# Kernel optimization log

Hardware: AMD Instinct MI355X
Metric: run time of the kernel (lower is better)

Reference implementation:

```python
import jax, jax.numpy as jnp
import numpy as np

N = 2048       # x_dim (input features)
M = 2048       # y_dim (output features)
R0 = 1024      # components in table 0 (knn table)
D_K = 1024     # key encoder embed dim
D_V = 1024     # val encoder embed dim
BATCH = 512
ISTA_ALPHA = 1.0
ISTA_MAXITER = 5


def _ortho_encoder(key, n, d):
    # get_embedding_matrix with ortho=True: QR of (s,s) gaussian, take [:n,:d]
    s = max(n, d)
    q = jnp.linalg.qr(jax.random.normal(key, (s, s), dtype=jnp.float32))[0]
    return q[:n, :d]


def setup_inputs() -> dict:
    key = jax.random.key(0)
    kw, kk, kv, kx = jax.random.split(key, 4)
    W = jax.random.normal(kw, (N, M), dtype=jnp.float32) / np.float32(np.sqrt(N))
    # torch: V, S, U = svd(W); U = U.T  -> V = left vecs (n,k), U = right vecs (m,k)
    Usvd, S, Vh = jnp.linalg.svd(W, full_matrices=False)
    V = Usvd          # (n, k)
    Ur = Vh.T         # (m, k)
    key_enc = _ortho_encoder(kk, N, D_K)   # (n, d_k)
    val_enc = _ortho_encoder(kv, M, D_V)   # (m, d_v)
    # table 0: knn table over components [0:R0]
    keys_t0 = V[:, :R0].T @ key_enc        # (R0, d_k)
    vals_t0 = Ur[:, :R0].T @ val_enc       # (R0, d_v)
    scales_t0 = S[:R0][:, None]            # (R0, 1)
    # table 1: plain low-rank table over components [R0:]
    keys_t1 = V[:, R0:]                    # (n, R1)
    vals_t1 = Ur[:, R0:]                   # (m, R1)
    scales_t1 = S[R0:][:, None]            # (R1, 1)
    x = jax.random.normal(kx, (BATCH, N), dtype=jnp.float32)
    return {"x": x, "key_enc": key_enc, "val_enc": val_enc,
            "keys_t0": keys_t0, "vals_t0": vals_t0, "scales_t0": scales_t0,
            "keys_t1": keys_t1, "vals_t1": vals_t1, "scales_t1": scales_t1}


def _soft(x, t):
    return jnp.sign(x) * jnp.maximum(jnp.abs(x) - t, 0.0)


def reference(x, key_enc, val_enc, keys_t0, vals_t0, scales_t0,
              keys_t1, vals_t1, scales_t1):
    # --- table 0: knn path (batched; original looped over batch samples) ---
    q = x @ key_enc                        # (B, d_k)
    alphas = q @ keys_t0.T                 # (B, R0)
    betas = alphas * scales_t0.T           # (B, R0)
    yb = betas @ vals_t0                   # (B, d_v)
    # ISTA: min ||yb - z @ val_enc||^2 + alpha*||z||_1, step=1 (val_enc has
    # orthonormal columns so Lipschitz const of grad is 1)
    z = yb @ val_enc.T                     # z0, (B, m)
    for _ in range(ISTA_MAXITER):
        z = _soft(z + (yb - z @ val_enc) @ val_enc.T, ISTA_ALPHA)
    y = z                                  # knn path assigns y[b,:] = yh
    # --- table 1: low-rank path (accumulates) ---
    alphas2 = x @ keys_t1                  # (B, R1)
    betas2 = alphas2 * scales_t1.T         # (B, R1)
    y = y + betas2 @ vals_t1.T             # (B, m)
    return y
```

## Files before the change

kernel.cpp:

```cpp
#include <hip/hip_runtime.h>


typedef _Float16 f16x8 __attribute__((ext_vector_type(8)));
typedef _Float16 f16x4 __attribute__((ext_vector_type(4)));
typedef float f32x4 __attribute__((ext_vector_type(4)));

enum { EPI_H, EPI_QOFF, EPI_SPLIT, EPI_SOFT, EPI_ZQ, EPI_ZQF, EPI_FINAL };

typedef const __attribute__((address_space(1))) void* gas_ptr;
typedef __attribute__((address_space(3))) void* las_ptr;

__device__ __forceinline__ void gload16(const void* g, void* l) {
  __builtin_amdgcn_global_load_lds((gas_ptr)g, (las_ptr)l, 16, 0, 0);
}

__device__ __forceinline__ float softt(float t) {
  float s = fabsf(t) - 1.0f;
  s = s > 0.0f ? s : 0.0f;
  return copysignf(s, t);
}

__global__ __launch_bounds__(256) void convAll(
    const float* __restrict__ e0, const float* __restrict__ e1,
    const float* __restrict__ e2, const float* __restrict__ e3,
    _Float16* __restrict__ o0, _Float16* __restrict__ o1,
    _Float16* __restrict__ o2, _Float16* __restrict__ o3,
    const float* __restrict__ s1, const float* __restrict__ s2,
    const float4* __restrict__ pa, f16x4* __restrict__ qa, int na,
    const float4* __restrict__ pb, f16x4* __restrict__ qb, int nb,
    const float4* __restrict__ pc, f16x4* __restrict__ qc, int nc) {
  const int z = blockIdx.z;
  if (z == 4) {
    const int total = na + nb + nc;
    const int bid = blockIdx.y * 32 + blockIdx.x;
    const int nthr = 2048 * 256;
    for (int i = bid * 256 + threadIdx.y * 32 + threadIdx.x; i < total;
         i += nthr) {
      const float4* s;
      f16x4* d;
      int j = i;
      if (j < na) {
        s = pa; d = qa;
      } else if ((j -= na) < nb) {
        s = pb; d = qb;
      } else {
        j -= nb; s = pc; d = qc;
      }
      float4 v = s[j];
      f16x4 h = {(_Float16)v.x, (_Float16)v.y, (_Float16)v.z, (_Float16)v.w};
      d[j] = h;
    }
    return;
  }
  const float* in = z == 0 ? e0 : z == 1 ? e1 : z == 2 ? e2 : e3;
  _Float16* out = z == 0 ? o0 : z == 1 ? o1 : z == 2 ? o2 : o3;
  const int R = (z < 2) ? 2048 : 1024;
  const int C = 1024;
  const int mode = z == 1 ? 1 : z == 2 ? 2 : 0;
  const float* sv = z == 1 ? s1 : s2;
  __shared__ float t[32][33];
  const int tx = threadIdx.x, ty = threadIdx.y;
  const int c0 = blockIdx.x * 32, r0 = blockIdx.y * 32;
  if (r0 >= R) return;
#pragma unroll
  for (int i = 0; i < 32; i += 8)
    t[ty + i][tx] = in[(size_t)(r0 + ty + i) * C + c0 + tx];
  __syncthreads();
#pragma unroll
  for (int i = 0; i < 32; i += 8) {
    float v = t[tx][ty + i];
    if (mode == 1) v *= sv[c0 + ty + i];
    if (mode == 2) v *= sv[r0 + tx];
    out[(size_t)(c0 + ty + i) * R + r0 + tx] = (_Float16)v;
  }
}

template <int EPI>
__device__ __forceinline__ void gtile(
    const _Float16* __restrict__ A, int lda, const _Float16* __restrict__ B,
    int ldb, int nK, int N, int brow, int bcol, const float* __restrict__ dgv,
    float* __restrict__ dgout, float* __restrict__ fA, float* __restrict__ fB,
    _Float16* __restrict__ oh, _Float16* __restrict__ oh2,
    float* __restrict__ ofin, _Float16* sm, int tid) {
  const int lane = tid & 63;
  const int w = tid >> 6;
  const int wr = w & 1;
  const int wk = w >> 1;
  const int srow = lane >> 3;
  const int scol = ((lane & 7) ^ srow) << 3;
  const int a15 = lane & 15;
  const int hi = lane >> 4;
  const int l7 = lane & 7;

  const _Float16* apg = A + (size_t)(brow + (w << 4) + srow) * lda + scol;
  const _Float16* bpg = B + (size_t)(bcol + (w << 4) + srow) * ldb + scol;
  _Float16* AB = sm;
  _Float16* BB = sm + 16384;
  const int ldstA = w << 10;

  const int ca = ((wk << 2) + hi) ^ l7;
  int raddr[2], baddr[4];
#pragma unroll
  for (int mi = 0; mi < 2; ++mi)
    raddr[mi] = ((wr << 5) + (mi << 4) + a15) * 64 + (ca << 3);
#pragma unroll
  for (int ni = 0; ni < 4; ++ni)
    baddr[ni] = ((ni << 4) + a15) * 64 + (ca << 3);

  f32x4 acc[2][4] = {};

  __syncthreads();

#pragma unroll
  for (int p = 0; p < 2; ++p) {
    gload16(apg + p * 64, AB + p * 4096 + ldstA);
    gload16(apg + p * 64 + (size_t)8 * lda, AB + p * 4096 + ldstA + 512);
    gload16(bpg + p * 64, BB + p * 4096 + ldstA);
    gload16(bpg + p * 64 + (size_t)8 * ldb, BB + p * 4096 + ldstA + 512);
  }

  for (int kt = 0; kt < nK; ++kt) {
    if (kt + 2 < nK) {
      const int bf = (kt + 2) & 3;
      const int co = (kt + 2) << 6;
      gload16(apg + co, AB + bf * 4096 + ldstA);
      gload16(apg + co + (size_t)8 * lda, AB + bf * 4096 + ldstA + 512);
      gload16(bpg + co, BB + bf * 4096 + ldstA);
      gload16(bpg + co + (size_t)8 * ldb, BB + bf * 4096 + ldstA + 512);
    }
    const int rem = nK - 1 - kt;
    if (rem >= 2)
      asm volatile("s_waitcnt vmcnt(8)" ::: "memory");
    else if (rem == 1)
      asm volatile("s_waitcnt vmcnt(4)" ::: "memory");
    else
      asm volatile("s_waitcnt vmcnt(0)" ::: "memory");
    __builtin_amdgcn_s_barrier();
    __builtin_amdgcn_sched_barrier(0);
    const _Float16* Ab = AB + (kt & 3) * 4096;
    const _Float16* Bb = BB + (kt & 3) * 4096;
    f16x8 av[2], bv[4];
    av[0] = *(const f16x8*)(Ab + raddr[0]);
    av[1] = *(const f16x8*)(Ab + raddr[1]);
    bv[0] = *(const f16x8*)(Bb + baddr[0]);
    bv[1] = *(const f16x8*)(Bb + baddr[1]);
    bv[2] = *(const f16x8*)(Bb + baddr[2]);
    bv[3] = *(const f16x8*)(Bb + baddr[3]);
#pragma unroll
    for (int mi = 0; mi < 2; ++mi)
#pragma unroll
      for (int ni = 0; ni < 4; ++ni)
        acc[mi][ni] = __builtin_amdgcn_mfma_f32_16x16x32_f16(
            av[mi], bv[ni], acc[mi][ni], 0, 0, 0);
  }

  __syncthreads();
  float* scr = (float*)sm;
  const int sl = (wr << 6) + lane;
  if (wk == 1) {
#pragma unroll
    for (int mi = 0; mi < 2; ++mi)
#pragma unroll
      for (int ni = 0; ni < 4; ++ni)
#pragma unroll
        for (int r = 0; r < 4; ++r)
          scr[(((mi << 2) + ni) * 4 + r) * 128 + sl] = acc[mi][ni][r];
  }
  __syncthreads();
  if (wk == 0) {
#pragma unroll
    for (int mi = 0; mi < 2; ++mi) {
#pragma unroll
      for (int ni = 0; ni < 4; ++ni) {
#pragma unroll
        for (int r = 0; r < 4; ++r) {
          const float v =
              acc[mi][ni][r] + scr[(((mi << 2) + ni) * 4 + r) * 128 + sl];
          const int row = brow + (wr << 5) + (mi << 4) + (hi << 2) + r;
          const int col = bcol + (ni << 4) + a15;
          const size_t idx = (size_t)row * N + col;
          if constexpr (EPI == EPI_H) {
            oh[idx] = (_Float16)v;
          } else if constexpr (EPI == EPI_QOFF) {
            if (row == col) {
              dgout[row] = 1.0f - v;
              oh[idx] = (_Float16)0.0f;
            } else {
              oh[idx] = (_Float16)(-v);
            }
          } else if constexpr (EPI == EPI_SPLIT) {
            if (col < 1024)
              oh[(size_t)row * 1024 + col] = (_Float16)v;
            else
              oh2[(size_t)row * 1024 + (col - 1024)] = (_Float16)v;
          } else if constexpr (EPI == EPI_SOFT) {
            fA[idx] = v;
            float s = softt(v);
            fB[idx] = s;
            oh[idx] = (_Float16)s;
          } else if constexpr (EPI == EPI_ZQ) {
            float t = fA[idx] + dgv[col] * fB[idx] + v;
            float s = softt(t);
            fB[idx] = s;
            oh[idx] = (_Float16)s;
          } else if constexpr (EPI == EPI_ZQF) {
            float t = fA[idx] + dgv[col] * fB[idx] + v;
            fB[idx] = softt(t);
          } else {
            ofin[idx] = fB[idx] + v;
          }
        }
      }
    }
  }
}

struct WS {
  const _Float16 *ve, *vt1, *w0pT_r, *Bcat, *qoff_r, *x, *kt0s, *vt0T, *w0_r,
      *q_r, *be2;
  _Float16 *w0pT_w, *qoff_w, *w0_w, *q_w, *be2_w, *zhA, *zhB;
  float *z0, *zf, *dg;
};

__global__ __launch_bounds__(256, 2) void kD2(WS p) {
  __shared__ __align__(16) _Float16 sm[32768];
  const int tid = threadIdx.x;
  const int bid = blockIdx.x;
  if (bid < 1024) {
    gtile<EPI_QOFF>(p.ve, 1024, p.ve, 1024, 16, 2048, (bid >> 5) << 6,
                    (bid & 31) << 6, nullptr, p.dg, nullptr, nullptr, p.qoff_w,
                    nullptr, nullptr, sm, tid);
  } else if (bid < 1280) {
    const int i = bid - 1024;
    gtile<EPI_SPLIT>(p.x, 2048, p.Bcat, 2048, 32, 2048, (i >> 5) << 6,
                     (i & 31) << 6, nullptr, nullptr, nullptr, nullptr, p.q_w,
                     p.be2_w, nullptr, sm, tid);
  } else {
    const int i = bid - 1280;
    gtile<EPI_H>(p.kt0s, 1024, p.vt0T, 1024, 16, 1024, (i >> 4) << 6,
                 (i & 15) << 6, nullptr, nullptr, nullptr, nullptr, p.w0_w,
                 nullptr, nullptr, sm, tid);
  }
}

__global__ __launch_bounds__(256, 2) void kW0p(WS p) {
  __shared__ __align__(16) _Float16 sm[32768];
  const int bid = blockIdx.x;
  gtile<EPI_H>(p.ve, 1024, p.w0_r, 1024, 16, 1024, (bid >> 4) << 6,
               (bid & 15) << 6, nullptr, nullptr, nullptr, nullptr, p.w0pT_w,
               nullptr, nullptr, sm, threadIdx.x);
}

__global__ __launch_bounds__(256, 2) void kC2(WS p) {
  __shared__ __align__(16) _Float16 sm[32768];
  const int bid = blockIdx.x;
  gtile<EPI_SOFT>(p.q_r, 1024, p.w0pT_r, 1024, 16, 2048, (bid >> 5) << 6,
                  (bid & 31) << 6, nullptr, nullptr, p.z0, p.zf, p.zhA,
                  nullptr, nullptr, sm, threadIdx.x);
}

template <bool AB>
__global__ __launch_bounds__(256, 2) void kZQ(WS p) {
  __shared__ __align__(16) _Float16 sm[32768];
  const int bid = blockIdx.x;
  gtile<EPI_ZQ>(AB ? p.zhA : p.zhB, 2048, p.qoff_r, 2048, 32, 2048,
                (bid >> 5) << 6, (bid & 31) << 6, p.dg, nullptr, p.z0, p.zf,
                AB ? p.zhB : p.zhA, nullptr, nullptr, sm, threadIdx.x);
}

__global__ __launch_bounds__(256, 2) void kZQF(WS p, float* out) {
  __shared__ __align__(16) _Float16 sm[32768];
  const int bid = blockIdx.x;
  const int brow = (bid >> 5) << 6, bcol = (bid & 31) << 6;
  gtile<EPI_ZQF>(p.zhB, 2048, p.qoff_r, 2048, 32, 2048, brow, bcol, p.dg,
                 nullptr, p.z0, p.zf, nullptr, nullptr, nullptr, sm,
                 threadIdx.x);
  gtile<EPI_FINAL>(p.be2, 1024, p.vt1, 1024, 16, 2048, brow, bcol, nullptr,
                   nullptr, nullptr, p.zf, nullptr, nullptr, out, sm,
                   threadIdx.x);
}

extern "C" void kernel_launch(void* const* d_in, const int* in_sizes, int n_in,
                              void* d_out, int out_size, void* d_ws,
                              size_t ws_size, hipStream_t stream) {
  const float* x = (const float*)d_in[0];
  const float* key_enc = (const float*)d_in[1];
  const float* val_enc = (const float*)d_in[2];
  const float* keys_t0 = (const float*)d_in[3];
  const float* vals_t0 = (const float*)d_in[4];
  const float* scales_t0 = (const float*)d_in[5];
  const float* keys_t1 = (const float*)d_in[6];
  const float* vals_t1 = (const float*)d_in[7];
  const float* scales_t1 = (const float*)d_in[8];

  constexpr size_t M1 = 1048576;
  _Float16* ws = (_Float16*)d_ws;
  _Float16* ve_h = ws;
  _Float16* vt1_h = ws + 2 * M1;
  _Float16* w0pT = ws + 4 * M1;
  _Float16* Bcat = ws + 6 * M1;
  _Float16* zhA = ws + 6 * M1;
  float* z0_f = (float*)(ws + 7 * M1);
  _Float16* zhB = ws + 9 * M1;
  _Float16* qoff = ws + 10 * M1;
  _Float16* x_h = ws + 14 * M1;
  _Float16* kt0s = ws + 15 * M1;
  float* z_f = (float*)(ws + 15 * M1);
  _Float16* vt0T = ws + 16 * M1;
  _Float16* w0 = ws + 17 * M1;
  _Float16* q_h = ws + 18 * M1;
  _Float16* be2 = ws + 18 * M1 + 524288;
  float* dg = (float*)(ws + 19 * M1);

  WS p;
  p.ve = ve_h; p.vt1 = vt1_h; p.w0pT_r = w0pT; p.w0pT_w = w0pT;
  p.Bcat = Bcat; p.qoff_r = qoff; p.qoff_w = qoff; p.x = x_h;
  p.kt0s = kt0s; p.vt0T = vt0T; p.w0_r = w0; p.w0_w = w0;
  p.q_r = q_h; p.q_w = q_h; p.be2 = be2; p.be2_w = be2;
  p.zhA = zhA; p.zhB = zhB; p.z0 = z0_f; p.zf = z_f; p.dg = dg;

  convAll<<<dim3(32, 64, 5), dim3(32, 8), 0, stream>>>(
      key_enc, keys_t1, keys_t0, vals_t0, Bcat, Bcat + 2 * M1, kt0s, vt0T,
      scales_t1, scales_t0, (const float4*)x, (f16x4*)x_h, 262144,
      (const float4*)val_enc, (f16x4*)ve_h, 524288, (const float4*)vals_t1,
      (f16x4*)vt1_h, 524288);
  kD2<<<1536, 256, 0, stream>>>(p);
  kW0p<<<512, 256, 0, stream>>>(p);
  kC2<<<256, 256, 0, stream>>>(p);
  kZQ<true><<<256, 256, 0, stream>>>(p);
  kZQ<false><<<256, 256, 0, stream>>>(p);
  kZQ<true><<<256, 256, 0, stream>>>(p);
  kZQF<<<256, 256, 0, stream>>>(p, (float*)d_out);
}
```

Baseline: 120.7 us.

## Replace precomputed Gram and weight products with factored low-rank ISTA chain

```diff
diff --git a/kernel.cpp b/kernel.cpp
--- a/kernel.cpp
+++ b/kernel.cpp
@@ -5,7 +5,7 @@
 typedef _Float16 f16x4 __attribute__((ext_vector_type(4)));
 typedef float f32x4 __attribute__((ext_vector_type(4)));
 
-enum { EPI_H, EPI_QOFF, EPI_SPLIT, EPI_SOFT, EPI_ZQ, EPI_ZQF, EPI_FINAL };
+enum { EPI_SPLIT, EPI_BH, EPI_YP, EPI_SOFT, EPI_ZUP, EPI_ZUPF };
 
 typedef const __attribute__((address_space(1))) void* gas_ptr;
 typedef __attribute__((address_space(3))) void* las_ptr;
@@ -21,193 +21,177 @@
 }
 
 __global__ __launch_bounds__(256) void convAll(
-    const float* __restrict__ e0, const float* __restrict__ e1,
-    const float* __restrict__ e2, const float* __restrict__ e3,
-    _Float16* __restrict__ o0, _Float16* __restrict__ o1,
-    _Float16* __restrict__ o2, _Float16* __restrict__ o3,
-    const float* __restrict__ s1, const float* __restrict__ s2,
-    const float4* __restrict__ pa, f16x4* __restrict__ qa, int na,
-    const float4* __restrict__ pb, f16x4* __restrict__ qb, int nb,
-    const float4* __restrict__ pc, f16x4* __restrict__ qc, int nc) {
+    const float* __restrict__ ke, const float* __restrict__ k1,
+    const float* __restrict__ v0, const float* __restrict__ ve,
+    _Float16* __restrict__ oKe, _Float16* __restrict__ oK1,
+    _Float16* __restrict__ oV0, _Float16* __restrict__ oVeT,
+    const float* __restrict__ s1, const float* __restrict__ s0,
+    const float4* __restrict__ px, f16x4* __restrict__ qx,
+    const float4* __restrict__ pve, f16x4* __restrict__ qve,
+    const float4* __restrict__ pv1, f16x4* __restrict__ qv1,
+    const float4* __restrict__ pk0, f16x4* __restrict__ qk0) {
   const int z = blockIdx.z;
   if (z == 4) {
-    const int total = na + nb + nc;
+    const int n_x = 262144, n_ve = 524288, n_v1 = 524288, n_k0 = 262144;
+    const int total = n_x + n_ve + n_v1 + n_k0;
     const int bid = blockIdx.y * 32 + blockIdx.x;
-    const int nthr = 2048 * 256;
     for (int i = bid * 256 + threadIdx.y * 32 + threadIdx.x; i < total;
-         i += nthr) {
+         i += 2048 * 256) {
+      int j = i;
       const float4* s;
       f16x4* d;
-      int j = i;
-      if (j < na) {
-        s = pa; d = qa;
-      } else if ((j -= na) < nb) {
-        s = pb; d = qb;
+      float sc = 1.0f;
+      if (j < n_x) {
+        s = px; d = qx;
+      } else if ((j -= n_x) < n_ve) {
+        s = pve; d = qve;
+      } else if ((j -= n_ve) < n_v1) {
+        s = pv1; d = qv1;
       } else {
-        j -= nb; s = pc; d = qc;
+        j -= n_v1; s = pk0; d = qk0; sc = s0[j >> 8];
       }
       float4 v = s[j];
-      f16x4 h = {(_Float16)v.x, (_Float16)v.y, (_Float16)v.z, (_Float16)v.w};
+      f16x4 h = {(_Float16)(v.x * sc), (_Float16)(v.y * sc),
+                 (_Float16)(v.z * sc), (_Float16)(v.w * sc)};
       d[j] = h;
     }
     return;
   }
-  const float* in = z == 0 ? e0 : z == 1 ? e1 : z == 2 ? e2 : e3;
-  _Float16* out = z == 0 ? o0 : z == 1 ? o1 : z == 2 ? o2 : o3;
-  const int R = (z < 2) ? 2048 : 1024;
-  const int C = 1024;
-  const int mode = z == 1 ? 1 : z == 2 ? 2 : 0;
-  const float* sv = z == 1 ? s1 : s2;
+  const float* in = z == 0 ? ke : z == 1 ? k1 : z == 2 ? v0 : ve;
+  _Float16* out = z == 0 ? oKe : z == 1 ? oK1 : z == 2 ? oV0 : oVeT;
+  const int R = (z == 2) ? 1024 : 2048;
+  const int mode = (z == 1) ? 1 : 0;
   __shared__ float t[32][33];
   const int tx = threadIdx.x, ty = threadIdx.y;
   const int c0 = blockIdx.x * 32, r0 = blockIdx.y * 32;
   if (r0 >= R) return;
 #pragma unroll
   for (int i = 0; i < 32; i += 8)
-    t[ty + i][tx] = in[(size_t)(r0 + ty + i) * C + c0 + tx];
+    t[ty + i][tx] = in[(size_t)(r0 + ty + i) * 1024 + c0 + tx];
   __syncthreads();
 #pragma unroll
   for (int i = 0; i < 32; i += 8) {
     float v = t[tx][ty + i];
-    if (mode == 1) v *= sv[c0 + ty + i];
-    if (mode == 2) v *= sv[r0 + tx];
+    if (mode == 1) v *= s1[c0 + ty + i];
     out[(size_t)(c0 + ty + i) * R + r0 + tx] = (_Float16)v;
   }
 }
 
 template <int EPI>
-__device__ __forceinline__ void gtile(
+__device__ __forceinline__ void gt32(
     const _Float16* __restrict__ A, int lda, const _Float16* __restrict__ B,
-    int ldb, int nK, int N, int brow, int bcol, const float* __restrict__ dgv,
-    float* __restrict__ dgout, float* __restrict__ fA, float* __restrict__ fB,
-    _Float16* __restrict__ oh, _Float16* __restrict__ oh2,
+    int ldb, int nK, int N, int brow, int bcol, float* __restrict__ fA,
+    float* __restrict__ fB, _Float16* __restrict__ oh,
+    _Float16* __restrict__ oh2, const float* __restrict__ fC,
     float* __restrict__ ofin, _Float16* sm, int tid) {
   const int lane = tid & 63;
   const int w = tid >> 6;
-  const int wr = w & 1;
+  const int wc = w & 1;
   const int wk = w >> 1;
   const int srow = lane >> 3;
   const int scol = ((lane & 7) ^ srow) << 3;
-  const int a15 = lane & 15;
-  const int hi = lane >> 4;
-  const int l7 = lane & 7;
-
-  const _Float16* apg = A + (size_t)(brow + (w << 4) + srow) * lda + scol;
+  const int a15 = lane & 15, hi = lane >> 4, l7 = lane & 7;
+
+  const _Float16* apg = A + (size_t)(brow + (w << 3) + srow) * lda + scol;
   const _Float16* bpg = B + (size_t)(bcol + (w << 4) + srow) * ldb + scol;
   _Float16* AB = sm;
-  _Float16* BB = sm + 16384;
-  const int ldstA = w << 10;
-
+  _Float16* BB = sm + 8192;
   const int ca = ((wk << 2) + hi) ^ l7;
-  int raddr[2], baddr[4];
+  int raddr[2], baddr[2];
 #pragma unroll
   for (int mi = 0; mi < 2; ++mi)
-    raddr[mi] = ((wr << 5) + (mi << 4) + a15) * 64 + (ca << 3);
-#pragma unroll
-  for (int ni = 0; ni < 4; ++ni)
-    baddr[ni] = ((ni << 4) + a15) * 64 + (ca << 3);
-
-  f32x4 acc[2][4] = {};
-
+    raddr[mi] = ((mi << 4) + a15) * 64 + (ca << 3);
+#pragma unroll
+  for (int ni = 0; ni < 2; ++ni)
+    baddr[ni] = ((wc << 5) + (ni << 4) + a15) * 64 + (ca << 3);
+
+  f32x4 acc[2][2] = {};
   __syncthreads();
 
 #pragma unroll
   for (int p = 0; p < 2; ++p) {
-    gload16(apg + p * 64, AB + p * 4096 + ldstA);
-    gload16(apg + p * 64 + (size_t)8 * lda, AB + p * 4096 + ldstA + 512);
-    gload16(bpg + p * 64, BB + p * 4096 + ldstA);
-    gload16(bpg + p * 64 + (size_t)8 * ldb, BB + p * 4096 + ldstA + 512);
-  }
-
+    gload16(apg + p * 64, AB + p * 2048 + (w << 9));
+    gload16(bpg + p * 64, BB + p * 4096 + (w << 10));
+    gload16(bpg + p * 64 + (size_t)8 * ldb, BB + p * 4096 + (w << 10) + 512);
+  }
   for (int kt = 0; kt < nK; ++kt) {
     if (kt + 2 < nK) {
       const int bf = (kt + 2) & 3;
       const int co = (kt + 2) << 6;
-      gload16(apg + co, AB + bf * 4096 + ldstA);
-      gload16(apg + co + (size_t)8 * lda, AB + bf * 4096 + ldstA + 512);
-      gload16(bpg + co, BB + bf * 4096 + ldstA);
-      gload16(bpg + co + (size_t)8 * ldb, BB + bf * 4096 + ldstA + 512);
+      gload16(apg + co, AB + bf * 2048 + (w << 9));
+      gload16(bpg + co, BB + bf * 4096 + (w << 10));
+      gload16(bpg + co + (size_t)8 * ldb, BB + bf * 4096 + (w << 10) + 512);
     }
     const int rem = nK - 1 - kt;
     if (rem >= 2)
-      asm volatile("s_waitcnt vmcnt(8)" ::: "memory");
+      asm volatile("s_waitcnt vmcnt(6)" ::: "memory");
     else if (rem == 1)
-      asm volatile("s_waitcnt vmcnt(4)" ::: "memory");
+      asm volatile("s_waitcnt vmcnt(3)" ::: "memory");
     else
       asm volatile("s_waitcnt vmcnt(0)" ::: "memory");
     __builtin_amdgcn_s_barrier();
     __builtin_amdgcn_sched_barrier(0);
-    const _Float16* Ab = AB + (kt & 3) * 4096;
+    const _Float16* Ab = AB + (kt & 3) * 2048;
     const _Float16* Bb = BB + (kt & 3) * 4096;
-    f16x8 av[2], bv[4];
+    f16x8 av[2], bv[2];
     av[0] = *(const f16x8*)(Ab + raddr[0]);
     av[1] = *(const f16x8*)(Ab + raddr[1]);
     bv[0] = *(const f16x8*)(Bb + baddr[0]);
     bv[1] = *(const f16x8*)(Bb + baddr[1]);
-    bv[2] = *(const f16x8*)(Bb + baddr[2]);
-    bv[3] = *(const f16x8*)(Bb + baddr[3]);
 #pragma unroll
     for (int mi = 0; mi < 2; ++mi)
 #pragma unroll
-      for (int ni = 0; ni < 4; ++ni)
+      for (int ni = 0; ni < 2; ++ni)
         acc[mi][ni] = __builtin_amdgcn_mfma_f32_16x16x32_f16(
             av[mi], bv[ni], acc[mi][ni], 0, 0, 0);
   }
-
   __syncthreads();
   float* scr = (float*)sm;
-  const int sl = (wr << 6) + lane;
+  const int sl = (wc << 6) + lane;
   if (wk == 1) {
 #pragma unroll
     for (int mi = 0; mi < 2; ++mi)
 #pragma unroll
-      for (int ni = 0; ni < 4; ++ni)
+      for (int ni = 0; ni < 2; ++ni)
 #pragma unroll
         for (int r = 0; r < 4; ++r)
-          scr[(((mi << 2) + ni) * 4 + r) * 128 + sl] = acc[mi][ni][r];
+          scr[(((mi << 1) + ni) * 4 + r) * 128 + sl] = acc[mi][ni][r];
   }
   __syncthreads();
   if (wk == 0) {
 #pragma unroll
     for (int mi = 0; mi < 2; ++mi) {
 #pragma unroll
-      for (int ni = 0; ni < 4; ++ni) {
+      for (int ni = 0; ni < 2; ++ni) {
 #pragma unroll
         for (int r = 0; r < 4; ++r) {
           const float v =
-              acc[mi][ni][r] + scr[(((mi << 2) + ni) * 4 + r) * 128 + sl];
-          const int row = brow + (wr << 5) + (mi << 4) + (hi << 2) + r;
-          const int col = bcol + (ni << 4) + a15;
+              acc[mi][ni][r] + scr[(((mi << 1) + ni) * 4 + r) * 128 + sl];
+          const int row = brow + (mi << 4) + (hi << 2) + r;
+          const int col = bcol + (wc << 5) + (ni << 4) + a15;
           const size_t idx = (size_t)row * N + col;
-          if constexpr (EPI == EPI_H) {
-            oh[idx] = (_Float16)v;
-          } else if constexpr (EPI == EPI_QOFF) {
-            if (row == col) {
-              dgout[row] = 1.0f - v;
-              oh[idx] = (_Float16)0.0f;
-            } else {
-              oh[idx] = (_Float16)(-v);
-            }
-          } else if constexpr (EPI == EPI_SPLIT) {
+          if constexpr (EPI == EPI_SPLIT) {
             if (col < 1024)
               oh[(size_t)row * 1024 + col] = (_Float16)v;
             else
               oh2[(size_t)row * 1024 + (col - 1024)] = (_Float16)v;
+          } else if constexpr (EPI == EPI_BH) {
+            oh[idx] = (_Float16)v;
+          } else if constexpr (EPI == EPI_YP) {
+            ofin[idx] = v;
           } else if constexpr (EPI == EPI_SOFT) {
             fA[idx] = v;
             float s = softt(v);
             fB[idx] = s;
             oh[idx] = (_Float16)s;
-          } else if constexpr (EPI == EPI_ZQ) {
-            float t = fA[idx] + dgv[col] * fB[idx] + v;
+          } else if constexpr (EPI == EPI_ZUP) {
+            float t = fA[idx] + fB[idx] - v;
             float s = softt(t);
             fB[idx] = s;
             oh[idx] = (_Float16)s;
-          } else if constexpr (EPI == EPI_ZQF) {
-            float t = fA[idx] + dgv[col] * fB[idx] + v;
-            fB[idx] = softt(t);
           } else {
-            ofin[idx] = fB[idx] + v;
+            float t = fA[idx] + fB[idx] - v;
+            ofin[idx] = fC[idx] + softt(t);
           }
         }
       }
@@ -216,68 +200,93 @@
 }
 
 struct WS {
-  const _Float16 *ve, *vt1, *w0pT_r, *Bcat, *qoff_r, *x, *kt0s, *vt0T, *w0_r,
-      *q_r, *be2;
-  _Float16 *w0pT_w, *qoff_w, *w0_w, *q_w, *be2_w, *zhA, *zhB;
-  float *z0, *zf, *dg;
+  const _Float16 *ve, *veT, *vt1, *Bcat, *x, *k0r, *vt0T, *q_r, *be2_r,
+      *bet_r, *yb_r;
+  _Float16 *q_w, *be2_w, *bet_w, *yb_w, *c_w, *zhA, *zhB;
+  const _Float16* c_r;
+  float *z0, *zf, *yp;
 };
 
-__global__ __launch_bounds__(256, 2) void kD2(WS p) {
-  __shared__ __align__(16) _Float16 sm[32768];
-  const int tid = threadIdx.x;
+__device__ __forceinline__ void map512(int b, int& br, int& bc) {
+  const int x = b & 7, i = b >> 3;
+  bc = (x << 2) | (i & 3);
+  br = i >> 2;
+}
+__device__ __forceinline__ void map256(int b, int& br, int& bc) {
+  const int x = b & 7, i = b >> 3;
+  bc = (x << 1) | (i & 1);
+  br = i >> 1;
+}
+
+__global__ __launch_bounds__(256, 2) void kC1(WS p) {
+  __shared__ __align__(16) _Float16 sm[24576];
+  int br, bc;
+  map512(blockIdx.x, br, bc);
+  gt32<EPI_SPLIT>(p.x, 2048, p.Bcat, 2048, 32, 2048, br << 5, bc << 6,
+                  nullptr, nullptr, p.q_w, p.be2_w, nullptr, nullptr, sm,
+                  threadIdx.x);
+}
+
+__global__ __launch_bounds__(256, 2) void kBYP(WS p) {
+  __shared__ __align__(16) _Float16 sm[24576];
   const int bid = blockIdx.x;
-  if (bid < 1024) {
-    gtile<EPI_QOFF>(p.ve, 1024, p.ve, 1024, 16, 2048, (bid >> 5) << 6,
-                    (bid & 31) << 6, nullptr, p.dg, nullptr, nullptr, p.qoff_w,
-                    nullptr, nullptr, sm, tid);
-  } else if (bid < 1280) {
-    const int i = bid - 1024;
-    gtile<EPI_SPLIT>(p.x, 2048, p.Bcat, 2048, 32, 2048, (i >> 5) << 6,
-                     (i & 31) << 6, nullptr, nullptr, nullptr, nullptr, p.q_w,
-                     p.be2_w, nullptr, sm, tid);
+  int br, bc;
+  if (bid < 256) {
+    map256(bid, br, bc);
+    gt32<EPI_BH>(p.q_r, 1024, p.k0r, 1024, 16, 1024, br << 5, bc << 6,
+                 nullptr, nullptr, p.bet_w, nullptr, nullptr, nullptr, sm,
+                 threadIdx.x);
   } else {
-    const int i = bid - 1280;
-    gtile<EPI_H>(p.kt0s, 1024, p.vt0T, 1024, 16, 1024, (i >> 4) << 6,
-                 (i & 15) << 6, nullptr, nullptr, nullptr, nullptr, p.w0_w,
-                 nullptr, nullptr, sm, tid);
-  }
-}
-
-__global__ __launch_bounds__(256, 2) void kW0p(WS p) {
-  __shared__ __align__(16) _Float16 sm[32768];
-  const int bid = blockIdx.x;
-  gtile<EPI_H>(p.ve, 1024, p.w0_r, 1024, 16, 1024, (bid >> 4) << 6,
-               (bid & 15) << 6, nullptr, nullptr, nullptr, nullptr, p.w0pT_w,
-               nullptr, nullptr, sm, threadIdx.x);
-}
-
-__global__ __launch_bounds__(256, 2) void kC2(WS p) {
-  __shared__ __align__(16) _Float16 sm[32768];
-  const int bid = blockIdx.x;
-  gtile<EPI_SOFT>(p.q_r, 1024, p.w0pT_r, 1024, 16, 2048, (bid >> 5) << 6,
-                  (bid & 31) << 6, nullptr, nullptr, p.z0, p.zf, p.zhA,
-                  nullptr, nullptr, sm, threadIdx.x);
+    map512(bid - 256, br, bc);
+    gt32<EPI_YP>(p.be2_r, 1024, p.vt1, 1024, 16, 2048, br << 5, bc << 6,
+                 nullptr, nullptr, nullptr, nullptr, nullptr, p.yp, sm,
+                 threadIdx.x);
+  }
+}
+
+__global__ __launch_bounds__(256, 2) void kYB(WS p) {
+  __shared__ __align__(16) _Float16 sm[24576];
+  int br, bc;
+  map256(blockIdx.x, br, bc);
+  gt32<EPI_BH>(p.bet_r, 1024, p.vt0T, 1024, 16, 1024, br << 5, bc << 6,
+               nullptr, nullptr, p.yb_w, nullptr, nullptr, nullptr, sm,
+               threadIdx.x);
+}
+
+__global__ __launch_bounds__(256, 2) void kZ0(WS p) {
+  __shared__ __align__(16) _Float16 sm[24576];
+  int br, bc;
+  map512(blockIdx.x, br, bc);
+  gt32<EPI_SOFT>(p.yb_r, 1024, p.ve, 1024, 16, 2048, br << 5, bc << 6, p.z0,
+                 p.zf, p.zhA, nullptr, nullptr, nullptr, sm, threadIdx.x);
 }
 
 template <bool AB>
-__global__ __launch_bounds__(256, 2) void kZQ(WS p) {
-  __shared__ __align__(16) _Float16 sm[32768];
-  const int bid = blockIdx.x;
-  gtile<EPI_ZQ>(AB ? p.zhA : p.zhB, 2048, p.qoff_r, 2048, 32, 2048,
-                (bid >> 5) << 6, (bid & 31) << 6, p.dg, nullptr, p.z0, p.zf,
-                AB ? p.zhB : p.zhA, nullptr, nullptr, sm, threadIdx.x);
-}
-
-__global__ __launch_bounds__(256, 2) void kZQF(WS p, float* out) {
-  __shared__ __align__(16) _Float16 sm[32768];
-  const int bid = blockIdx.x;
-  const int brow = (bid >> 5) << 6, bcol = (bid & 31) << 6;
-  gtile<EPI_ZQF>(p.zhB, 2048, p.qoff_r, 2048, 32, 2048, brow, bcol, p.dg,
-                 nullptr, p.z0, p.zf, nullptr, nullptr, nullptr, sm,
-                 threadIdx.x);
-  gtile<EPI_FINAL>(p.be2, 1024, p.vt1, 1024, 16, 2048, brow, bcol, nullptr,
-                   nullptr, nullptr, p.zf, nullptr, nullptr, out, sm,
-                   threadIdx.x);
+__global__ __launch_bounds__(256, 2) void kC(WS p) {
+  __shared__ __align__(16) _Float16 sm[24576];
+  int br, bc;
+  map256(blockIdx.x, br, bc);
+  gt32<EPI_BH>(AB ? p.zhA : p.zhB, 2048, p.veT, 2048, 32, 1024, br << 5,
+               bc << 6, nullptr, nullptr, p.c_w, nullptr, nullptr, nullptr,
+               sm, threadIdx.x);
+}
+
+template <bool AB>
+__global__ __launch_bounds__(256, 2) void kZU(WS p) {
+  __shared__ __align__(16) _Float16 sm[24576];
+  int br, bc;
+  map512(blockIdx.x, br, bc);
+  gt32<EPI_ZUP>(p.c_r, 1024, p.ve, 1024, 16, 2048, br << 5, bc << 6, p.z0,
+                p.zf, AB ? p.zhB : p.zhA, nullptr, nullptr, nullptr, sm,
+                threadIdx.x);
+}
+
+__global__ __launch_bounds__(256, 2) void kZUF(WS p, float* out) {
+  __shared__ __align__(16) _Float16 sm[24576];
+  int br, bc;
+  map512(blockIdx.x, br, bc);
+  gt32<EPI_ZUPF>(p.c_r, 1024, p.ve, 1024, 16, 2048, br << 5, bc << 6, p.z0,
+                 p.zf, nullptr, nullptr, p.yp, out, sm, threadIdx.x);
 }
 
 extern "C" void kernel_launch(void* const* d_in, const int* in_sizes, int n_in,
@@ -296,39 +305,45 @@
   constexpr size_t M1 = 1048576;
   _Float16* ws = (_Float16*)d_ws;
   _Float16* ve_h = ws;
-  _Float16* vt1_h = ws + 2 * M1;
-  _Float16* w0pT = ws + 4 * M1;
+  _Float16* veT = ws + 2 * M1;
+  _Float16* vt1_h = ws + 4 * M1;
   _Float16* Bcat = ws + 6 * M1;
   _Float16* zhA = ws + 6 * M1;
   float* z0_f = (float*)(ws + 7 * M1);
   _Float16* zhB = ws + 9 * M1;
-  _Float16* qoff = ws + 10 * M1;
-  _Float16* x_h = ws + 14 * M1;
-  _Float16* kt0s = ws + 15 * M1;
+  _Float16* x_h = ws + 10 * M1;
+  _Float16* k0r = ws + 11 * M1;
+  _Float16* c_h = ws + 11 * M1;
+  _Float16* vt0T = ws + 12 * M1;
+  _Float16* q_h = ws + 13 * M1;
+  _Float16* be2 = ws + 13 * M1 + 524288;
+  _Float16* bet_h = ws + 14 * M1;
+  _Float16* yb_h = ws + 14 * M1 + 524288;
   float* z_f = (float*)(ws + 15 * M1);
-  _Float16* vt0T = ws + 16 * M1;
-  _Float16* w0 = ws + 17 * M1;
-  _Float16* q_h = ws + 18 * M1;
-  _Float16* be2 = ws + 18 * M1 + 524288;
-  float* dg = (float*)(ws + 19 * M1);
+  float* yp = (float*)(ws + 17 * M1);
 
   WS p;
-  p.ve = ve_h; p.vt1 = vt1_h; p.w0pT_r = w0pT; p.w0pT_w = w0pT;
-  p.Bcat = Bcat; p.qoff_r = qoff; p.qoff_w = qoff; p.x = x_h;
-  p.kt0s = kt0s; p.vt0T = vt0T; p.w0_r = w0; p.w0_w = w0;
-  p.q_r = q_h; p.q_w = q_h; p.be2 = be2; p.be2_w = be2;
-  p.zhA = zhA; p.zhB = zhB; p.z0 = z0_f; p.zf = z_f; p.dg = dg;
+  p.ve = ve_h; p.veT = veT; p.vt1 = vt1_h; p.Bcat = Bcat; p.x = x_h;
+  p.k0r = k0r; p.vt0T = vt0T; p.q_r = q_h; p.q_w = q_h;
+  p.be2_r = be2; p.be2_w = be2; p.bet_r = bet_h; p.bet_w = bet_h;
+  p.yb_r = yb_h; p.yb_w = yb_h; p.c_r = c_h; p.c_w = c_h;
+  p.zhA = zhA; p.zhB = zhB; p.z0 = z0_f; p.zf = z_f; p.yp = yp;
 
   convAll<<<dim3(32, 64, 5), dim3(32, 8), 0, stream>>>(
-      key_enc, keys_t1, keys_t0, vals_t0, Bcat, Bcat + 2 * M1, kt0s, vt0T,
-      scales_t1, scales_t0, (const float4*)x, (f16x4*)x_h, 262144,
-      (const float4*)val_enc, (f16x4*)ve_h, 524288, (const float4*)vals_t1,
-      (f16x4*)vt1_h, 524288);
-  kD2<<<1536, 256, 0, stream>>>(p);
-  kW0p<<<512, 256, 0, stream>>>(p);
-  kC2<<<256, 256, 0, stream>>>(p);
-  kZQ<true><<<256, 256, 0, stream>>>(p);
-  kZQ<false><<<256, 256, 0, stream>>>(p);
-  kZQ<true><<<256, 256, 0, stream>>>(p);
-  kZQF<<<256, 256, 0, stream>>>(p, (float*)d_out);
-}
+      key_enc, keys_t1, vals_t0, val_enc, Bcat, Bcat + 2 * M1, vt0T, veT,
+      scales_t1, scales_t0, (const float4*)x, (f16x4*)x_h,
+      (const float4*)val_enc, (f16x4*)ve_h, (const float4*)vals_t1,
+      (f16x4*)vt1_h, (const float4*)keys_t0, (f16x4*)k0r);
+  kC1<<<512, 256, 0, stream>>>(p);
+  kBYP<<<768, 256, 0, stream>>>(p);
+  kYB<<<256, 256, 0, stream>>>(p);
+  kZ0<<<512, 256, 0, stream>>>(p);
+  kC<true><<<256, 256, 0, stream>>>(p);
+  kZU<true><<<512, 256, 0, stream>>>(p);
+  kC<false><<<256, 256, 0, stream>>>(p);
+  kZU<false><<<512, 256, 0, stream>>>(p);
+  kC<true><<<256, 256, 0, stream>>>(p);
+  kZU<true><<<512, 256, 0, stream>>>(p);
+  kC<false><<<256, 256, 0, stream>>>(p);
+  kZUF<<<512, 256, 0, stream>>>(p, (float*)d_out);
+}
```

Result: faster. 117.0 us (-3.1%).

## Shrink GEMM tiles to 32x32, swizzle block order, hoist low-rank GEMM earlier

Applied to the files above, without the earlier changes.

```diff
diff --git a/kernel.cpp b/kernel.cpp
--- a/kernel.cpp
+++ b/kernel.cpp
@@ -5,7 +5,7 @@
 typedef _Float16 f16x4 __attribute__((ext_vector_type(4)));
 typedef float f32x4 __attribute__((ext_vector_type(4)));
 
-enum { EPI_H, EPI_QOFF, EPI_SPLIT, EPI_SOFT, EPI_ZQ, EPI_ZQF, EPI_FINAL };
+enum { EPI_H, EPI_QOFF, EPI_SPLIT, EPI_SOFT, EPI_YP, EPI_ZQ, EPI_ZQFO };
 
 typedef const __attribute__((address_space(1))) void* gas_ptr;
 typedef __attribute__((address_space(3))) void* las_ptr;
@@ -76,57 +76,54 @@
 }
 
 template <int EPI>
-__device__ __forceinline__ void gtile(
+__device__ __forceinline__ void g2w(
     const _Float16* __restrict__ A, int lda, const _Float16* __restrict__ B,
-    int ldb, int nK, int N, int brow, int bcol, const float* __restrict__ dgv,
-    float* __restrict__ dgout, float* __restrict__ fA, float* __restrict__ fB,
+    int ldb, int nK, int N, int brow, int bcol,
+    const float* __restrict__ dgv, float* __restrict__ dgout,
+    float* __restrict__ fA, float* __restrict__ fB,
     _Float16* __restrict__ oh, _Float16* __restrict__ oh2,
-    float* __restrict__ ofin, _Float16* sm, int tid) {
+    const float* __restrict__ fC, float* __restrict__ ofin, _Float16* sm,
+    int tid) {
   const int lane = tid & 63;
   const int w = tid >> 6;
-  const int wr = w & 1;
-  const int wk = w >> 1;
   const int srow = lane >> 3;
   const int scol = ((lane & 7) ^ srow) << 3;
-  const int a15 = lane & 15;
-  const int hi = lane >> 4;
-  const int l7 = lane & 7;
+  const int a15 = lane & 15, hi = lane >> 4, l7 = lane & 7;
 
   const _Float16* apg = A + (size_t)(brow + (w << 4) + srow) * lda + scol;
   const _Float16* bpg = B + (size_t)(bcol + (w << 4) + srow) * ldb + scol;
   _Float16* AB = sm;
-  _Float16* BB = sm + 16384;
-  const int ldstA = w << 10;
-
-  const int ca = ((wk << 2) + hi) ^ l7;
-  int raddr[2], baddr[4];
+  _Float16* BB = sm + 8192;
+  const int wdst = w << 10;
+
+  const int ca = ((w << 2) + hi) ^ l7;
+  int raddr[2], baddr[2];
 #pragma unroll
   for (int mi = 0; mi < 2; ++mi)
-    raddr[mi] = ((wr << 5) + (mi << 4) + a15) * 64 + (ca << 3);
-#pragma unroll
-  for (int ni = 0; ni < 4; ++ni)
+    raddr[mi] = ((mi << 4) + a15) * 64 + (ca << 3);
+#pragma unroll
+  for (int ni = 0; ni < 2; ++ni)
     baddr[ni] = ((ni << 4) + a15) * 64 + (ca << 3);
 
-  f32x4 acc[2][4] = {};
-
-  __syncthreads();
+  f32x4 acc[2][2] = {};
 
 #pragma unroll
   for (int p = 0; p < 2; ++p) {
-    gload16(apg + p * 64, AB + p * 4096 + ldstA);
-    gload16(apg + p * 64 + (size_t)8 * lda, AB + p * 4096 + ldstA + 512);
-    gload16(bpg + p * 64, BB + p * 4096 + ldstA);
-    gload16(bpg + p * 64 + (size_t)8 * ldb, BB + p * 4096 + ldstA + 512);
+    const int co = p << 6;
+    gload16(apg + co, AB + p * 2048 + wdst);
+    gload16(apg + co + (size_t)8 * lda, AB + p * 2048 + wdst + 512);
+    gload16(bpg + co, BB + p * 2048 + wdst);
+    gload16(bpg + co + (size_t)8 * ldb, BB + p * 2048 + wdst + 512);
   }
 
   for (int kt = 0; kt < nK; ++kt) {
     if (kt + 2 < nK) {
       const int bf = (kt + 2) & 3;
       const int co = (kt + 2) << 6;
-      gload16(apg + co, AB + bf * 4096 + ldstA);
-      gload16(apg + co + (size_t)8 * lda, AB + bf * 4096 + ldstA + 512);
-      gload16(bpg + co, BB + bf * 4096 + ldstA);
-      gload16(bpg + co + (size_t)8 * ldb, BB + bf * 4096 + ldstA + 512);
+      gload16(apg + co, AB + bf * 2048 + wdst);
+      gload16(apg + co + (size_t)8 * lda, AB + bf * 2048 + wdst + 512);
+      gload16(bpg + co, BB + bf * 2048 + wdst);
+      gload16(bpg + co + (size_t)8 * ldb, BB + bf * 2048 + wdst + 512);
     }
     const int rem = nK - 1 - kt;
     if (rem >= 2)
@@ -137,78 +134,74 @@
       asm volatile("s_waitcnt vmcnt(0)" ::: "memory");
     __builtin_amdgcn_s_barrier();
     __builtin_amdgcn_sched_barrier(0);
-    const _Float16* Ab = AB + (kt & 3) * 4096;
-    const _Float16* Bb = BB + (kt & 3) * 4096;
-    f16x8 av[2], bv[4];
+    const _Float16* Ab = AB + (kt & 3) * 2048;
+    const _Float16* Bb = BB + (kt & 3) * 2048;
+    f16x8 av[2], bv[2];
     av[0] = *(const f16x8*)(Ab + raddr[0]);
     av[1] = *(const f16x8*)(Ab + raddr[1]);
     bv[0] = *(const f16x8*)(Bb + baddr[0]);
     bv[1] = *(const f16x8*)(Bb + baddr[1]);
-    bv[2] = *(const f16x8*)(Bb + baddr[2]);
-    bv[3] = *(const f16x8*)(Bb + baddr[3]);
 #pragma unroll
     for (int mi = 0; mi < 2; ++mi)
 #pragma unroll
-      for (int ni = 0; ni < 4; ++ni)
+      for (int ni = 0; ni < 2; ++ni)
         acc[mi][ni] = __builtin_amdgcn_mfma_f32_16x16x32_f16(
             av[mi], bv[ni], acc[mi][ni], 0, 0, 0);
   }
 
   __syncthreads();
   float* scr = (float*)sm;
-  const int sl = (wr << 6) + lane;
-  if (wk == 1) {
+  if (w == 1) {
 #pragma unroll
     for (int mi = 0; mi < 2; ++mi)
 #pragma unroll
-      for (int ni = 0; ni < 4; ++ni)
+      for (int ni = 0; ni < 2; ++ni)
 #pragma unroll
         for (int r = 0; r < 4; ++r)
-          scr[(((mi << 2) + ni) * 4 + r) * 128 + sl] = acc[mi][ni][r];
+          scr[(((mi << 1) + ni) * 4 + r) * 64 + lane] = acc[mi][ni][r];
   }
   __syncthreads();
-  if (wk == 0) {
-#pragma unroll
-    for (int mi = 0; mi < 2; ++mi) {
-#pragma unroll
-      for (int ni = 0; ni < 4; ++ni) {
-#pragma unroll
-        for (int r = 0; r < 4; ++r) {
-          const float v =
-              acc[mi][ni][r] + scr[(((mi << 2) + ni) * 4 + r) * 128 + sl];
-          const int row = brow + (wr << 5) + (mi << 4) + (hi << 2) + r;
-          const int col = bcol + (ni << 4) + a15;
-          const size_t idx = (size_t)row * N + col;
-          if constexpr (EPI == EPI_H) {
-            oh[idx] = (_Float16)v;
-          } else if constexpr (EPI == EPI_QOFF) {
-            if (row == col) {
-              dgout[row] = 1.0f - v;
-              oh[idx] = (_Float16)0.0f;
-            } else {
-              oh[idx] = (_Float16)(-v);
-            }
-          } else if constexpr (EPI == EPI_SPLIT) {
-            if (col < 1024)
-              oh[(size_t)row * 1024 + col] = (_Float16)v;
-            else
-              oh2[(size_t)row * 1024 + (col - 1024)] = (_Float16)v;
-          } else if constexpr (EPI == EPI_SOFT) {
-            fA[idx] = v;
-            float s = softt(v);
-            fB[idx] = s;
-            oh[idx] = (_Float16)s;
-          } else if constexpr (EPI == EPI_ZQ) {
-            float t = fA[idx] + dgv[col] * fB[idx] + v;
-            float s = softt(t);
-            fB[idx] = s;
-            oh[idx] = (_Float16)s;
-          } else if constexpr (EPI == EPI_ZQF) {
-            float t = fA[idx] + dgv[col] * fB[idx] + v;
-            fB[idx] = softt(t);
+  if (w != 0) return;
+#pragma unroll
+  for (int mi = 0; mi < 2; ++mi) {
+#pragma unroll
+    for (int ni = 0; ni < 2; ++ni) {
+#pragma unroll
+      for (int r = 0; r < 4; ++r) {
+        const float v =
+            acc[mi][ni][r] + scr[(((mi << 1) + ni) * 4 + r) * 64 + lane];
+        const int row = brow + (mi << 4) + (hi << 2) + r;
+        const int col = bcol + (ni << 4) + a15;
+        const size_t idx = (size_t)row * N + col;
+        if constexpr (EPI == EPI_H) {
+          oh[idx] = (_Float16)v;
+        } else if constexpr (EPI == EPI_QOFF) {
+          if (row == col) {
+            dgout[row] = 1.0f - v;
+            oh[idx] = (_Float16)0.0f;
           } else {
-            ofin[idx] = fB[idx] + v;
+            oh[idx] = (_Float16)(-v);
           }
+        } else if constexpr (EPI == EPI_SPLIT) {
+          if (col < 1024)
+            oh[(size_t)row * 1024 + col] = (_Float16)v;
+          else
+            oh2[(size_t)row * 1024 + (col - 1024)] = (_Float16)v;
+        } else if constexpr (EPI == EPI_SOFT) {
+          fA[idx] = v;
+          float s = softt(v);
+          fB[idx] = s;
+          oh[idx] = (_Float16)s;
+        } else if constexpr (EPI == EPI_YP) {
+          ofin[idx] = v;
+        } else if constexpr (EPI == EPI_ZQ) {
+          float t = fA[idx] + dgv[col] * fB[idx] + v;
+          float s = softt(t);
+          fB[idx] = s;
+          oh[idx] = (_Float16)s;
+        } else {
+          float t = fA[idx] + dgv[col] * fB[idx] + v;
+          ofin[idx] = fC[idx] + softt(t);
         }
       }
     }
@@ -219,65 +212,86 @@
   const _Float16 *ve, *vt1, *w0pT_r, *Bcat, *qoff_r, *x, *kt0s, *vt0T, *w0_r,
       *q_r, *be2;
   _Float16 *w0pT_w, *qoff_w, *w0_w, *q_w, *be2_w, *zhA, *zhB;
-  float *z0, *zf, *dg;
+  float *z0, *zf, *dg, *yp;
 };
 
-__global__ __launch_bounds__(256, 2) void kD2(WS p) {
-  __shared__ __align__(16) _Float16 sm[32768];
+__device__ __forceinline__ void map64(int b, int& br, int& bc) {
+  const int x = b & 7, j = b >> 3;
+  bc = (x << 3) | (j & 7);
+  br = j >> 3;
+}
+__device__ __forceinline__ void map32c(int b, int& br, int& bc) {
+  const int x = b & 7, j = b >> 3;
+  bc = (x << 2) | (j & 3);
+  br = j >> 2;
+}
+
+__global__ __launch_bounds__(128, 2) void kD2(WS p) {
+  __shared__ __align__(16) _Float16 sm[16384];
   const int tid = threadIdx.x;
   const int bid = blockIdx.x;
+  int br, bc;
+  if (bid < 4096) {
+    map64(bid, br, bc);
+    g2w<EPI_QOFF>(p.ve, 1024, p.ve, 1024, 16, 2048, br << 5, bc << 5,
+                  nullptr, p.dg, nullptr, nullptr, p.qoff_w, nullptr, nullptr,
+                  nullptr, sm, tid);
+  } else if (bid < 5120) {
+    map64(bid - 4096, br, bc);
+    g2w<EPI_SPLIT>(p.x, 2048, p.Bcat, 2048, 32, 2048, br << 5, bc << 5,
+                   nullptr, nullptr, nullptr, nullptr, p.q_w, p.be2_w,
+                   nullptr, nullptr, sm, tid);
+  } else {
+    map32c(bid - 5120, br, bc);
+    g2w<EPI_H>(p.kt0s, 1024, p.vt0T, 1024, 16, 1024, br << 5, bc << 5,
+               nullptr, nullptr, nullptr, nullptr, p.w0_w, nullptr, nullptr,
+               nullptr, sm, tid);
+  }
+}
+
+__global__ __launch_bounds__(128, 2) void kW0p(WS p) {
+  __shared__ __align__(16) _Float16 sm[16384];
+  int br, bc;
+  map32c(blockIdx.x, br, bc);
+  g2w<EPI_H>(p.ve, 1024, p.w0_r, 1024, 16, 1024, br << 5, bc << 5, nullptr,
+             nullptr, nullptr, nullptr, p.w0pT_w, nullptr, nullptr, nullptr,
+             sm, threadIdx.x);
+}
+
+__global__ __launch_bounds__(128, 2) void kD4(WS p) {
+  __shared__ __align__(16) _Float16 sm[16384];
+  const int bid = blockIdx.x;
+  int br, bc;
   if (bid < 1024) {
-    gtile<EPI_QOFF>(p.ve, 1024, p.ve, 1024, 16, 2048, (bid >> 5) << 6,
-                    (bid & 31) << 6, nullptr, p.dg, nullptr, nullptr, p.qoff_w,
-                    nullptr, nullptr, sm, tid);
-  } else if (bid < 1280) {
-    const int i = bid - 1024;
-    gtile<EPI_SPLIT>(p.x, 2048, p.Bcat, 2048, 32, 2048, (i >> 5) << 6,
-                     (i & 31) << 6, nullptr, nullptr, nullptr, nullptr, p.q_w,
-                     p.be2_w, nullptr, sm, tid);
+    map64(bid, br, bc);
+    g2w<EPI_SOFT>(p.q_r, 1024, p.w0pT_r, 1024, 16, 2048, br << 5, bc << 5,
+                  nullptr, nullptr, p.z0, p.zf, p.zhA, nullptr, nullptr,
+                  nullptr, sm, threadIdx.x);
   } else {
-    const int i = bid - 1280;
-    gtile<EPI_H>(p.kt0s, 1024, p.vt0T, 1024, 16, 1024, (i >> 4) << 6,
-                 (i & 15) << 6, nullptr, nullptr, nullptr, nullptr, p.w0_w,
-                 nullptr, nullptr, sm, tid);
-  }
-}
-
-__global__ __launch_bounds__(256, 2) void kW0p(WS p) {
-  __shared__ __align__(16) _Float16 sm[32768];
-  const int bid = blockIdx.x;
-  gtile<EPI_H>(p.ve, 1024, p.w0_r, 1024, 16, 1024, (bid >> 4) << 6,
-               (bid & 15) << 6, nullptr, nullptr, nullptr, nullptr, p.w0pT_w,
-               nullptr, nullptr, sm, threadIdx.x);
-}
-
-__global__ __launch_bounds__(256, 2) void kC2(WS p) {
-  __shared__ __align__(16) _Float16 sm[32768];
-  const int bid = blockIdx.x;
-  gtile<EPI_SOFT>(p.q_r, 1024, p.w0pT_r, 1024, 16, 2048, (bid >> 5) << 6,
-                  (bid & 31) << 6, nullptr, nullptr, p.z0, p.zf, p.zhA,
-                  nullptr, nullptr, sm, threadIdx.x);
+    map64(bid - 1024, br, bc);
+    g2w<EPI_YP>(p.be2, 1024, p.vt1, 1024, 16, 2048, br << 5, bc << 5,
+                nullptr, nullptr, nullptr, nullptr, nullptr, nullptr, nullptr,
+                p.yp, sm, threadIdx.x);
+  }
 }
 
 template <bool AB>
-__global__ __launch_bounds__(256, 2) void kZQ(WS p) {
-  __shared__ __align__(16) _Float16 sm[32768];
-  const int bid = blockIdx.x;
-  gtile<EPI_ZQ>(AB ? p.zhA : p.zhB, 2048, p.qoff_r, 2048, 32, 2048,
-                (bid >> 5) << 6, (bid & 31) << 6, p.dg, nullptr, p.z0, p.zf,
-                AB ? p.zhB : p.zhA, nullptr, nullptr, sm, threadIdx.x);
-}
-
-__global__ __launch_bounds__(256, 2) void kZQF(WS p, float* out) {
-  __shared__ __align__(16) _Float16 sm[32768];
-  const int bid = blockIdx.x;
-  const int brow = (bid >> 5) << 6, bcol = (bid & 31) << 6;
-  gtile<EPI_ZQF>(p.zhB, 2048, p.qoff_r, 2048, 32, 2048, brow, bcol, p.dg,
-                 nullptr, p.z0, p.zf, nullptr, nullptr, nullptr, sm,
-                 threadIdx.x);
-  gtile<EPI_FINAL>(p.be2, 1024, p.vt1, 1024, 16, 2048, brow, bcol, nullptr,
-                   nullptr, nullptr, p.zf, nullptr, nullptr, out, sm,
-                   threadIdx.x);
+__global__ __launch_bounds__(128, 2) void kZQ(WS p) {
+  __shared__ __align__(16) _Float16 sm[16384];
+  int br, bc;
+  map64(blockIdx.x, br, bc);
+  g2w<EPI_ZQ>(AB ? p.zhA : p.zhB, 2048, p.qoff_r, 2048, 32, 2048, br << 5,
+              bc << 5, p.dg, nullptr, p.z0, p.zf, AB ? p.zhB : p.zhA,
+              nullptr, nullptr, nullptr, sm, threadIdx.x);
+}
+
+__global__ __launch_bounds__(128, 2) void kZQF(WS p, float* out) {
+  __shared__ __align__(16) _Float16 sm[16384];
+  int br, bc;
+  map64(blockIdx.x, br, bc);
+  g2w<EPI_ZQFO>(p.zhB, 2048, p.qoff_r, 2048, 32, 2048, br << 5, bc << 5,
+                p.dg, nullptr, p.z0, p.zf, nullptr, nullptr, p.yp, out, sm,
+                threadIdx.x);
 }
 
 extern "C" void kernel_launch(void* const* d_in, const int* in_sizes, int n_in,
@@ -296,6 +310,7 @@
   constexpr size_t M1 = 1048576;
   _Float16* ws = (_Float16*)d_ws;
   _Float16* ve_h = ws;
+  float* yp = (float*)ws;
   _Float16* vt1_h = ws + 2 * M1;
   _Float16* w0pT = ws + 4 * M1;
   _Float16* Bcat = ws + 6 * M1;
@@ -317,18 +332,18 @@
   p.Bcat = Bcat; p.qoff_r = qoff; p.qoff_w = qoff; p.x = x_h;
   p.kt0s = kt0s; p.vt0T = vt0T; p.w0_r = w0; p.w0_w = w0;
   p.q_r = q_h; p.q_w = q_h; p.be2 = be2; p.be2_w = be2;
-  p.zhA = zhA; p.zhB = zhB; p.z0 = z0_f; p.zf = z_f; p.dg = dg;
+  p.zhA = zhA; p.zhB = zhB; p.z0 = z0_f; p.zf = z_f; p.dg = dg; p.yp = yp;
 
   convAll<<<dim3(32, 64, 5), dim3(32, 8), 0, stream>>>(
       key_enc, keys_t1, keys_t0, vals_t0, Bcat, Bcat + 2 * M1, kt0s, vt0T,
       scales_t1, scales_t0, (const float4*)x, (f16x4*)x_h, 262144,
       (const float4*)val_enc, (f16x4*)ve_h, 524288, (const float4*)vals_t1,
       (f16x4*)vt1_h, 524288);
-  kD2<<<1536, 256, 0, stream>>>(p);
-  kW0p<<<512, 256, 0, stream>>>(p);
-  kC2<<<256, 256, 0, stream>>>(p);
-  kZQ<true><<<256, 256, 0, stream>>>(p);
-  kZQ<false><<<256, 256, 0, stream>>>(p);
-  kZQ<true><<<256, 256, 0, stream>>>(p);
-  kZQF<<<256, 256, 0, stream>>>(p, (float*)d_out);
-}
+  kD2<<<6144, 128, 0, stream>>>(p);
+  kW0p<<<2048, 128, 0, stream>>>(p);
+  kD4<<<2048, 128, 0, stream>>>(p);
+  kZQ<true><<<1024, 128, 0, stream>>>(p);
+  kZQ<false><<<1024, 128, 0, stream>>>(p);
+  kZQ<true><<<1024, 128, 0, stream>>>(p);
+  kZQF<<<1024, 128, 0, stream>>>(p, (float*)d_out);
+}
```

Result: slower. 136.0 us (+12.6%).
